# Optimization experiments

Measured on AMD Instinct MI355X. Metric: run time of the kernel, lower is better.

## Reference

```python
import jax, jax.numpy as jnp
import numpy as np

T, B, D, H = 512, 64, 512, 512

def setup_inputs() -> dict:
    key = jax.random.key(0)
    ks = jax.random.split(key, 14)
    s = 0.02
    inp = {
        "inputs": jax.random.normal(ks[0], (T, B, D), dtype=jnp.float32),
        # gate linears: weight [D+H, H] (transposed torch layout), bias [H]
        "Wf": jax.random.normal(ks[1], (D + H, H), dtype=jnp.float32) * s,
        "bf": jax.random.normal(ks[2], (H,), dtype=jnp.float32) * s,
        "Wi": jax.random.normal(ks[3], (D + H, H), dtype=jnp.float32) * s,
        "bi": jax.random.normal(ks[4], (H,), dtype=jnp.float32) * s,
        "Wg": jax.random.normal(ks[5], (D + H, H), dtype=jnp.float32) * s,
        "bg": jax.random.normal(ks[6], (H,), dtype=jnp.float32) * s,
        "Wo": jax.random.normal(ks[7], (D + H, H), dtype=jnp.float32) * s,
        "bo": jax.random.normal(ks[8], (H,), dtype=jnp.float32) * s,
        # residual linears on hidden state: [H, H], no bias
        "Rf": jax.random.normal(ks[9], (H, H), dtype=jnp.float32) * s,
        "Ri": jax.random.normal(ks[10], (H, H), dtype=jnp.float32) * s,
        "Rg": jax.random.normal(ks[11], (H, H), dtype=jnp.float32) * s,
        "Ro": jax.random.normal(ks[12], (H, H), dtype=jnp.float32) * s,
    }
    return inp


def reference(inputs, Wf, bf, Wi, bi, Wg, bg, Wo, bo, Rf, Ri, Rg, Ro):
    # QLSTM forward (eval mode, gate_dropout inactive). states=None -> zeros.
    batch = inputs.shape[1]
    hidden = Wf.shape[1]
    h0 = jnp.zeros((batch, hidden), dtype=inputs.dtype)
    c0 = jnp.zeros((batch, hidden), dtype=inputs.dtype)

    # Fuse the 4 gate GEMMs into one [D+H, 4H] matmul and the 4 residual
    # GEMMs into one [H, 4H] matmul (same math, fewer launches).
    W4 = jnp.concatenate([Wf, Wi, Wg, Wo], axis=1)   # [D+H, 4H]
    b4 = jnp.concatenate([bf, bi, bg, bo], axis=0)   # [4H]
    R4 = jnp.concatenate([Rf, Ri, Rg, Ro], axis=1)   # [H, 4H]

    def step(carry, x):
        hx, cx = carry
        combined = jnp.concatenate([x, hx], axis=1)            # [B, D+H]
        z = combined @ W4 + b4 + hx @ R4                        # [B, 4H]
        f, i, g, o = jnp.split(z, 4, axis=1)
        f = jax.nn.sigmoid(f)
        i = jax.nn.sigmoid(i)
        g = jnp.tanh(g)
        o = jax.nn.sigmoid(o)
        cx = f * cx + i * g
        hx = o * jnp.tanh(cx)
        return (hx, cx), hx

    (hx, cx), stacked = jax.lax.scan(step, (h0, c0), inputs)
    return stacked, hx, cx
```

## Files before the change

### kernel.cpp

```cpp
#include <hip/hip_runtime.h>
#include <hip/hip_bf16.h>

typedef __attribute__((ext_vector_type(8))) short s16x8;
typedef __attribute__((ext_vector_type(4))) float f32x4;

__device__ __forceinline__ ushort f2bf(float x) {
  __hip_bfloat16 b = __float2bfloat16(x);
  return *reinterpret_cast<ushort*>(&b);
}
__device__ __forceinline__ float bf2f(ushort u) {
  union { unsigned int i; float f; } c; c.i = ((unsigned int)u) << 16; return c.f;
}
__device__ __forceinline__ float sigm_fast(float z) {
  return __builtin_amdgcn_rcpf(1.0f + __builtin_amdgcn_exp2f(z * -1.44269504088896f));
}

__global__ __launch_bounds__(256) void pack_weights(
    const float* __restrict__ Wf, const float* __restrict__ Wi,
    const float* __restrict__ Wg, const float* __restrict__ Wo,
    const float* __restrict__ Rf, const float* __restrict__ Ri,
    const float* __restrict__ Rg, const float* __restrict__ Ro,
    const float* __restrict__ bfp, const float* __restrict__ bip,
    const float* __restrict__ bgp, const float* __restrict__ bop,
    ushort* __restrict__ Wx, ushort* __restrict__ Rs, float* __restrict__ bp)
{
  const int p = blockIdx.x * 8 + (threadIdx.x >> 5);
  const int kk = (threadIdx.x & 31) * 16;
  const int gate = p & 3;
  const int hcol = (p >> 5) * 8 + ((p >> 4) & 1) * 4 + ((p & 15) >> 2);
  const float* W = (gate == 0) ? Wf : (gate == 1) ? Wi : (gate == 2) ? Wg : Wo;
  const float* R = (gate == 0) ? Rf : (gate == 1) ? Ri : (gate == 2) ? Rg : Ro;
  union { ushort u[16]; s16x8 v[2]; } wb, rb;
#pragma unroll
  for (int e = 0; e < 16; ++e) {
    const int k = kk + e;
    wb.u[e] = f2bf(W[(size_t)k * 512 + hcol]);
    rb.u[e] = f2bf(W[(size_t)(512 + k) * 512 + hcol] + R[(size_t)k * 512 + hcol]);
  }
  *(s16x8*)(Wx + (size_t)p * 512 + kk)     = wb.v[0];
  *(s16x8*)(Wx + (size_t)p * 512 + kk + 8) = wb.v[1];
  *(s16x8*)(Rs + (size_t)p * 512 + kk)     = rb.v[0];
  *(s16x8*)(Rs + (size_t)p * 512 + kk + 8) = rb.v[1];
  if ((threadIdx.x & 31) == 0) {
    const float* B = (gate == 0) ? bfp : (gate == 1) ? bip : (gate == 2) ? bgp : bop;
    bp[p] = B[hcol];
  }
}

__global__ __launch_bounds__(512, 1) void fused_kernel(
    const float* __restrict__ x, const ushort* __restrict__ Wx,
    const ushort* __restrict__ Rs, const float* __restrict__ bp,
    const ushort* __restrict__ zxr, ushort* __restrict__ zxw,
    ushort* __restrict__ hbuf, float* __restrict__ csave,
    int* __restrict__ flags, ushort* __restrict__ hsave,
    float* __restrict__ cfinal, int t0, int CH, int zxt0, int do_rec)
{
  __shared__ ushort lds_u[33280];
  const int tid = threadIdx.x;
  const int wid = tid >> 6;
  const int lane = tid & 63;
  const int l15 = lane & 15;
  const int hi = lane >> 4;

  if (blockIdx.x >= 32) {
    if (zxt0 >= 512) return;
    const int zbid = blockIdx.x - 32;
    const int pg = zbid & 15;
    const int ts = zbid >> 4;
    const int mpair = wid >> 2;
    const int np = wid & 3;
    const int q = pg * 4 + np;
    s16x8 Bg[2][16];
#pragma unroll
    for (int nt = 0; nt < 2; ++nt)
#pragma unroll
      for (int kc = 0; kc < 16; ++kc)
        Bg[nt][kc] = *(const s16x8*)(Wx + (size_t)(q * 32 + nt * 16 + l15) * 512 + kc * 32 + hi * 8);
    const int tper = CH >> 3;
    for (int tt = 0; tt < tper; ++tt) {
      const int tl = ts * tper + tt;
      const int t = zxt0 + tl;
      const float4* x4 = (const float4*)(x + (size_t)t * 32768);
#pragma unroll
      for (int j = 0; j < 16; ++j) {
        const int i4 = j * 512 + tid;
        const float4 v = x4[i4];
        const int row = i4 >> 7;
        const int c0 = (i4 & 127) * 4;
        ushort4 u;
        u.x = f2bf(v.x); u.y = f2bf(v.y); u.z = f2bf(v.z); u.w = f2bf(v.w);
        *(ushort4*)(&lds_u[row * 520 + c0]) = u;
      }
      __syncthreads();
#pragma unroll
      for (int a = 0; a < 2; ++a) {
        const int mt = mpair * 2 + a;
        f32x4 a0 = {0.f, 0.f, 0.f, 0.f};
        f32x4 a1 = {0.f, 0.f, 0.f, 0.f};
#pragma unroll
        for (int kc = 0; kc < 16; ++kc) {
          const s16x8 af = *(const s16x8*)(&lds_u[(mt * 16 + l15) * 520 + kc * 32 + hi * 8]);
          a0 = __builtin_amdgcn_mfma_f32_16x16x32_bf16(af, Bg[0][kc], a0, 0, 0, 0);
          a1 = __builtin_amdgcn_mfma_f32_16x16x32_bf16(af, Bg[1][kc], a1, 0, 0, 0);
        }
        union { ushort u[8]; s16x8 v; } ub;
#pragma unroll
        for (int r = 0; r < 4; ++r) { ub.u[r] = f2bf(a0[r]); ub.u[4 + r] = f2bf(a1[r]); }
        *(s16x8*)(zxw + ((((size_t)tl * 4 + mt) * 64 + q) * 64 + lane) * 8) = ub.v;
      }
      __syncthreads();
    }
    return;
  }

  if (!do_rec) return;
  ushort* hsl = lds_u;
  ushort* tbuf = lds_u + 8192;
  const int bid = blockIdx.x;
  const int g = bid & 3;
  const int mem = bid >> 2;
  const int q = mem * 8 + wid;
  const int gate = lane & 3;

  f32x4 Brg[2][16];
#pragma unroll
  for (int nt = 0; nt < 2; ++nt)
#pragma unroll
    for (int kc = 0; kc < 16; ++kc) {
      Brg[nt][kc] = *(const f32x4*)(Rs + (size_t)(q * 32 + nt * 16 + l15) * 512 + kc * 32 + hi * 8);
      asm volatile("" : "+v"(Brg[nt][kc]));
    }
  const float b0 = bp[q * 32 + l15];
  const float b1 = bp[q * 32 + 16 + l15];

  float cst[2][4];
  float* csp = csave + ((size_t)(bid * 8 + wid) * 64 + lane) * 8;
  if (t0 == 0) {
#pragma unroll
    for (int i = 0; i < 2; ++i)
#pragma unroll
      for (int r = 0; r < 4; ++r) cst[i][r] = 0.0f;
  } else {
#pragma unroll
    for (int i = 0; i < 2; ++i)
#pragma unroll
      for (int r = 0; r < 4; ++r) cst[i][r] = csp[i * 4 + r];
  }

  const int srow = hi * 4 + gate;
  const int hcol0 = q * 8 + (l15 >> 2);
  const int crow = tid >> 5;
  const int cbyte = (tid & 31) * 32;
  const int cswz = (crow & 7) << 4;
  const int srcofs = crow * 512 + (cbyte >> 1);
  const int wofs0 = (crow * 1024 + (cbyte ^ cswz)) >> 1;
  const int wofs1 = (crow * 1024 + ((cbyte + 16) ^ cswz)) >> 1;
  const int abase = l15 * 1024 + hi * 16;
  const int aswz = (l15 & 7) << 4;
  int* const myflag = &flags[(g * 8 + mem) * 1024];
  int* const pollp = &flags[(g * 8 + (lane & 7)) * 1024];

  for (int tl = 0; tl < CH; ++tl) {
    const int t = t0 + tl;
    if (tl > 0) {
      asm volatile("s_waitcnt vmcnt(0)" ::: "memory");
      __syncthreads();
      if (tid == 0)
        __hip_atomic_store(myflag, t, __ATOMIC_RELAXED, __HIP_MEMORY_SCOPE_AGENT);
    }
    const s16x8 zv = *(const s16x8*)(zxr + ((((size_t)tl * 4 + g) * 64 + q) * 64 + lane) * 8);
    if (tl > 0) {
      int v = 0x7fffffff;
      if (lane < 8) v = __hip_atomic_load(pollp, __ATOMIC_RELAXED, __HIP_MEMORY_SCOPE_AGENT);
      while (!__all(v >= t)) {
        if (lane < 8) v = __hip_atomic_load(pollp, __ATOMIC_RELAXED, __HIP_MEMORY_SCOPE_AGENT);
      }
      asm volatile("" ::: "memory");
    }
    const ushort* hs = hbuf + ((size_t)tl * 4 + g) * 8192;
    const s16x8 h0 = *(const s16x8*)(hs + srcofs);
    const s16x8 h1 = *(const s16x8*)(hs + srcofs + 8);
    *(s16x8*)(&hsl[wofs0]) = h0;
    *(s16x8*)(&hsl[wofs1]) = h1;
    __syncthreads();
    f32x4 a0 = {0.f, 0.f, 0.f, 0.f};
    f32x4 a1 = {0.f, 0.f, 0.f, 0.f};
#pragma unroll
    for (int kc = 0; kc < 16; ++kc) {
      const s16x8 af = *(const s16x8*)(&hsl[((abase + kc * 64) ^ aswz) >> 1]);
      a0 = __builtin_amdgcn_mfma_f32_16x16x32_bf16(af, __builtin_bit_cast(s16x8, Brg[0][kc]), a0, 0, 0, 0);
      a1 = __builtin_amdgcn_mfma_f32_16x16x32_bf16(af, __builtin_bit_cast(s16x8, Brg[1][kc]), a1, 0, 0, 0);
    }
    float hv[2], cv[2];
#pragma unroll
    for (int nt = 0; nt < 2; ++nt) {
      float hr[4];
#pragma unroll
      for (int r = 0; r < 4; ++r) {
        float z = (nt ? a1[r] : a0[r]) + bf2f((ushort)zv[nt * 4 + r]) + (nt ? b1 : b0);
        const float zz = (gate == 2) ? z + z : z;
        const float s = sigm_fast(zz);
        const float act = (gate == 2) ? (s + s - 1.0f) : s;
        const int ai = __float_as_int(act);
        const float fv = __int_as_float(__builtin_amdgcn_mov_dpp(ai, 0x00, 0xF, 0xF, true));
        const float iv = __int_as_float(__builtin_amdgcn_mov_dpp(ai, 0x55, 0xF, 0xF, true));
        const float gv = __int_as_float(__builtin_amdgcn_mov_dpp(ai, 0xAA, 0xF, 0xF, true));
        const float ov = __int_as_float(__builtin_amdgcn_mov_dpp(ai, 0xFF, 0xF, 0xF, true));
        const float cn = fmaf(fv, cst[nt][r], iv * gv);
        cst[nt][r] = cn;
        const float s2 = sigm_fast(cn + cn);
        hr[r] = ov * (s2 + s2 - 1.0f);
      }
      hv[nt] = (gate == 0) ? hr[0] : (gate == 1) ? hr[1] : (gate == 2) ? hr[2] : hr[3];
      cv[nt] = (gate == 0) ? cst[nt][0] : (gate == 1) ? cst[nt][1]
             : (gate == 2) ? cst[nt][2] : cst[nt][3];
    }
    const ushort pb0 = f2bf(hv[0]), pb1 = f2bf(hv[1]);
    {
      ushort2 hp; hp.x = pb0; hp.y = pb1;
      *(ushort2*)(hsave + (((size_t)t * 4 + g) * 8 + mem) * 1024 + wid * 128 + lane * 2) = hp;
      if (t == 511) {
        float* cf = cfinal + (((size_t)(g * 8 + mem) * 8 + wid) * 64 + lane) * 2;
        cf[0] = cv[0]; cf[1] = cv[1];
      }
    }
    tbuf[wid * 128 + srow * 8 + (l15 >> 2)]     = pb0;
    tbuf[wid * 128 + srow * 8 + (l15 >> 2) + 4] = pb1;
    asm volatile("s_waitcnt lgkmcnt(0)" ::: "memory");
    __builtin_amdgcn_sched_barrier(0);
    if (tl != CH - 1) {
      if (lane < 16) {
        const unsigned long long* rp = (const unsigned long long*)&tbuf[wid * 128 + lane * 8];
        ushort* dst = hbuf + ((size_t)(tl + 1) * 4 + g) * 8192 + lane * 512 + q * 8;
        __hip_atomic_store((unsigned long long*)dst, rp[0],
                           __ATOMIC_RELAXED, __HIP_MEMORY_SCOPE_AGENT);
        __hip_atomic_store((unsigned long long*)(dst + 4), rp[1],
                           __ATOMIC_RELAXED, __HIP_MEMORY_SCOPE_AGENT);
      }
    } else {
      ushort* hn0 = hbuf + (size_t)g * 8192;
      hn0[srow * 512 + hcol0]     = pb0;
      hn0[srow * 512 + hcol0 + 4] = pb1;
    }
  }
#pragma unroll
  for (int i = 0; i < 2; ++i)
#pragma unroll
    for (int r = 0; r < 4; ++r) csp[i * 4 + r] = cst[i][r];
}

__global__ __launch_bounds__(256) void reorder_kernel(
    const ushort* __restrict__ hsave, const float* __restrict__ cfinal,
    float* __restrict__ dout)
{
  __shared__ ushort lds[8192];
  const int t = blockIdx.x;
  const int g = blockIdx.y;
  const int tid = threadIdx.x;
  const s16x8* src = (const s16x8*)(hsave + ((size_t)t * 4 + g) * 8192);
#pragma unroll
  for (int j = 0; j < 4; ++j) {
    const int i = j * 256 + tid;
    *(s16x8*)(&lds[i * 8]) = src[i];
  }
  __syncthreads();
  const int srow = tid >> 4;
  const int cb = (tid & 15) * 32;
  float buf[32];
#pragma unroll
  for (int cc = 0; cc < 32; ++cc) {
    const int col = cb + cc;
    const int q = col >> 3;
    const int memb = q >> 3;
    const int wd = q & 7;
    const int nt = (col >> 2) & 1;
    const int l15v = ((col & 3) << 2) | (srow & 3);
    const int lanev = ((srow >> 2) << 4) | l15v;
    buf[cc] = bf2f(lds[memb * 1024 + wd * 128 + lanev * 2 + nt]);
  }
  float* o = dout + (size_t)t * 32768 + (size_t)(g * 16 + srow) * 512 + cb;
#pragma unroll
  for (int j = 0; j < 8; ++j) *(float4*)(o + j * 4) = *(const float4*)(&buf[j * 4]);
  if (t == 511) {
    float* oh = dout + (size_t)16777216 + (size_t)(g * 16 + srow) * 512 + cb;
#pragma unroll
    for (int j = 0; j < 8; ++j) *(float4*)(oh + j * 4) = *(const float4*)(&buf[j * 4]);
    float cbuf[32];
#pragma unroll
    for (int cc = 0; cc < 32; ++cc) {
      const int col = cb + cc;
      const int q = col >> 3;
      const int memb = q >> 3;
      const int wd = q & 7;
      const int nt = (col >> 2) & 1;
      const int l15v = ((col & 3) << 2) | (srow & 3);
      const int lanev = ((srow >> 2) << 4) | l15v;
      cbuf[cc] = cfinal[(((size_t)(g * 8 + memb) * 8 + wd) * 64 + lanev) * 2 + nt];
    }
    float* oc = dout + (size_t)16809984 + (size_t)(g * 16 + srow) * 512 + cb;
#pragma unroll
    for (int j = 0; j < 8; ++j) *(float4*)(oc + j * 4) = *(const float4*)(&cbuf[j * 4]);
  }
}

extern "C" void kernel_launch(void* const* d_in, const int* in_sizes, int n_in,
                              void* d_out, int out_size, void* d_ws, size_t ws_size,
                              hipStream_t stream)
{
  const float* x   = (const float*)d_in[0];
  const float* Wf  = (const float*)d_in[1];
  const float* bfp = (const float*)d_in[2];
  const float* Wi  = (const float*)d_in[3];
  const float* bip = (const float*)d_in[4];
  const float* Wg  = (const float*)d_in[5];
  const float* bgp = (const float*)d_in[6];
  const float* Wo  = (const float*)d_in[7];
  const float* bop = (const float*)d_in[8];
  const float* Rf  = (const float*)d_in[9];
  const float* Ri  = (const float*)d_in[10];
  const float* Rg  = (const float*)d_in[11];
  const float* Ro  = (const float*)d_in[12];
  float* dout = (float*)d_out;
  char* ws = (char*)d_ws;

  const size_t o_Wx = 0;
  const size_t o_Rs = 2097152;
  const size_t o_bp = 4194304;
  const size_t o_z0 = o_bp + 8192;

  int CH = 64;
  for (;;) {
    const size_t need = o_z0 + 2 * (size_t)CH * 262144
                      + (size_t)(CH + 1) * 65536
                      + 524288 + 131072 + 33554432 + 131072;
    if (need <= ws_size || CH <= 8) break;
    CH >>= 1;
  }
  const size_t zsz  = (size_t)CH * 262144;
  const size_t o_z1 = o_z0 + zsz;
  const size_t o_hb = o_z1 + zsz;
  const size_t o_cs = o_hb + (size_t)(CH + 1) * 65536;
  const size_t o_fl = o_cs + 524288;
  const size_t o_hs = o_fl + 131072;
  const size_t o_cf = o_hs + 33554432;

  ushort* Wx   = (ushort*)(ws + o_Wx);
  ushort* Rs   = (ushort*)(ws + o_Rs);
  float*  bp   = (float*)(ws + o_bp);
  ushort* zx0  = (ushort*)(ws + o_z0);
  ushort* zx1  = (ushort*)(ws + o_z1);
  ushort* hb   = (ushort*)(ws + o_hb);
  float*  csv  = (float*)(ws + o_cs);
  int*    fl   = (int*)(ws + o_fl);
  ushort* hsv  = (ushort*)(ws + o_hs);
  float*  cfin = (float*)(ws + o_cf);

  pack_weights<<<256, 256, 0, stream>>>(Wf, Wi, Wg, Wo, Rf, Ri, Rg, Ro,
                                        bfp, bip, bgp, bop, Wx, Rs, bp);
  hipMemsetAsync(hb, 0, 65536, stream);
  hipMemsetAsync(fl, 0, 131072, stream);

  fused_kernel<<<160, 512, 0, stream>>>(x, Wx, Rs, bp, zx1, zx0, hb, csv, fl,
                                        hsv, cfin, 0, CH, 0, 0);
  const int nch = 512 / CH;
  for (int c = 0; c < nch; ++c) {
    const ushort* zr = (c & 1) ? zx1 : zx0;
    ushort* zw       = (c & 1) ? zx0 : zx1;
    fused_kernel<<<160, 512, 0, stream>>>(x, Wx, Rs, bp, zr, zw, hb, csv, fl,
                                          hsv, cfin, c * CH, CH, (c + 1) * CH, 1);
  }
  reorder_kernel<<<dim3(512, 4), 256, 0, stream>>>(hsv, cfin, dout);
}
```

Before: 1.715 ms.

## Process two batch groups per recurrent block, halving recurrent block count

Each recurrent block now handles two batch groups (A and B) in sequence each timestep, reusing the same register-resident recurrent weights. This drops the recurrent grid from 32 to 16 blocks. The aim is to interleave the two groups so the flag polling and latency of one group overlaps the compute of the other. The cost is twice the serial compute per block per step, plus two flag stores and two barriers per iteration.

```diff
diff --git a/kernel.cpp b/kernel.cpp
--- a/kernel.cpp
+++ b/kernel.cpp
@@ -62,9 +62,9 @@
   const int l15 = lane & 15;
   const int hi = lane >> 4;
 
-  if (blockIdx.x >= 32) {
+  if (blockIdx.x >= 16) {
     if (zxt0 >= 512) return;
-    const int zbid = blockIdx.x - 32;
+    const int zbid = blockIdx.x - 16;
     const int pg = zbid & 15;
     const int ts = zbid >> 4;
     const int mpair = wid >> 2;
@@ -114,11 +114,14 @@
   }
 
   if (!do_rec) return;
-  ushort* hsl = lds_u;
-  ushort* tbuf = lds_u + 8192;
+  ushort* hslA = lds_u;
+  ushort* hslB = lds_u + 8192;
+  ushort* tbuf = lds_u + 16384;
   const int bid = blockIdx.x;
-  const int g = bid & 3;
-  const int mem = bid >> 2;
+  const int team = bid >> 3;
+  const int mem = bid & 7;
+  const int gA = team * 2;
+  const int gB = team * 2 + 1;
   const int q = mem * 8 + wid;
   const int gate = lane & 3;
 
@@ -133,18 +136,18 @@
   const float b0 = bp[q * 32 + l15];
   const float b1 = bp[q * 32 + 16 + l15];
 
-  float cst[2][4];
-  float* csp = csave + ((size_t)(bid * 8 + wid) * 64 + lane) * 8;
+  float cA[2][4], cB[2][4];
+  float* csp = csave + ((size_t)(bid * 8 + wid) * 64 + lane) * 16;
   if (t0 == 0) {
 #pragma unroll
     for (int i = 0; i < 2; ++i)
 #pragma unroll
-      for (int r = 0; r < 4; ++r) cst[i][r] = 0.0f;
+      for (int r = 0; r < 4; ++r) { cA[i][r] = 0.0f; cB[i][r] = 0.0f; }
   } else {
 #pragma unroll
     for (int i = 0; i < 2; ++i)
 #pragma unroll
-      for (int r = 0; r < 4; ++r) cst[i][r] = csp[i * 4 + r];
+      for (int r = 0; r < 4; ++r) { cA[i][r] = csp[i * 4 + r]; cB[i][r] = csp[8 + i * 4 + r]; }
   }
 
   const int srow = hi * 4 + gate;
@@ -157,96 +160,108 @@
   const int wofs1 = (crow * 1024 + ((cbyte + 16) ^ cswz)) >> 1;
   const int abase = l15 * 1024 + hi * 16;
   const int aswz = (l15 & 7) << 4;
-  int* const myflag = &flags[(g * 8 + mem) * 1024];
-  int* const pollp = &flags[(g * 8 + (lane & 7)) * 1024];
+  int* const myflagA = &flags[(gA * 8 + mem) * 1024];
+  int* const myflagB = &flags[(gB * 8 + mem) * 1024];
+  int* const pollA = &flags[(gA * 8 + (lane & 7)) * 1024];
+  int* const pollB = &flags[(gB * 8 + (lane & 7)) * 1024];
+
+#define SECTION(G, HSL, CST, POLLP)                                              \
+  {                                                                              \
+    const s16x8 zv = *(const s16x8*)(zxr + ((((size_t)tl * 4 + (G)) * 64 + q) * 64 + lane) * 8); \
+    if (tl > 0) {                                                                \
+      int v = 0x7fffffff;                                                        \
+      if (lane < 8) v = __hip_atomic_load(POLLP, __ATOMIC_RELAXED, __HIP_MEMORY_SCOPE_AGENT); \
+      while (!__all(v >= t)) {                                                   \
+        if (lane < 8) v = __hip_atomic_load(POLLP, __ATOMIC_RELAXED, __HIP_MEMORY_SCOPE_AGENT); \
+      }                                                                          \
+      asm volatile("" ::: "memory");                                             \
+    }                                                                            \
+    const ushort* hs_ = hbuf + ((size_t)tl * 4 + (G)) * 8192;                    \
+    const s16x8 h0_ = *(const s16x8*)(hs_ + srcofs);                             \
+    const s16x8 h1_ = *(const s16x8*)(hs_ + srcofs + 8);                         \
+    *(s16x8*)(&HSL[wofs0]) = h0_;                                                \
+    *(s16x8*)(&HSL[wofs1]) = h1_;                                                \
+    __syncthreads();                                                             \
+    f32x4 a0_ = {0.f, 0.f, 0.f, 0.f};                                            \
+    f32x4 a1_ = {0.f, 0.f, 0.f, 0.f};                                            \
+    _Pragma("unroll")                                                            \
+    for (int kc = 0; kc < 16; ++kc) {                                            \
+      const s16x8 af_ = *(const s16x8*)(&HSL[((abase + kc * 64) ^ aswz) >> 1]);  \
+      a0_ = __builtin_amdgcn_mfma_f32_16x16x32_bf16(af_, __builtin_bit_cast(s16x8, Brg[0][kc]), a0_, 0, 0, 0); \
+      a1_ = __builtin_amdgcn_mfma_f32_16x16x32_bf16(af_, __builtin_bit_cast(s16x8, Brg[1][kc]), a1_, 0, 0, 0); \
+    }                                                                            \
+    float hv_[2], cv_[2];                                                        \
+    _Pragma("unroll")                                                            \
+    for (int nt = 0; nt < 2; ++nt) {                                             \
+      float hr_[4];                                                              \
+      _Pragma("unroll")                                                          \
+      for (int r = 0; r < 4; ++r) {                                              \
+        float z = (nt ? a1_[r] : a0_[r]) + bf2f((ushort)zv[nt * 4 + r]) + (nt ? b1 : b0); \
+        const float zz = (gate == 2) ? z + z : z;                                \
+        const float s = sigm_fast(zz);                                           \
+        const float act = (gate == 2) ? (s + s - 1.0f) : s;                      \
+        const int ai = __float_as_int(act);                                      \
+        const float fv = __int_as_float(__builtin_amdgcn_mov_dpp(ai, 0x00, 0xF, 0xF, true)); \
+        const float iv = __int_as_float(__builtin_amdgcn_mov_dpp(ai, 0x55, 0xF, 0xF, true)); \
+        const float gv = __int_as_float(__builtin_amdgcn_mov_dpp(ai, 0xAA, 0xF, 0xF, true)); \
+        const float ov = __int_as_float(__builtin_amdgcn_mov_dpp(ai, 0xFF, 0xF, 0xF, true)); \
+        const float cn = fmaf(fv, CST[nt][r], iv * gv);                          \
+        CST[nt][r] = cn;                                                         \
+        const float s2 = sigm_fast(cn + cn);                                     \
+        hr_[r] = ov * (s2 + s2 - 1.0f);                                          \
+      }                                                                          \
+      hv_[nt] = (gate == 0) ? hr_[0] : (gate == 1) ? hr_[1] : (gate == 2) ? hr_[2] : hr_[3]; \
+      cv_[nt] = (gate == 0) ? CST[nt][0] : (gate == 1) ? CST[nt][1]              \
+              : (gate == 2) ? CST[nt][2] : CST[nt][3];                           \
+    }                                                                            \
+    const ushort pb0 = f2bf(hv_[0]), pb1 = f2bf(hv_[1]);                         \
+    {                                                                            \
+      ushort2 hp; hp.x = pb0; hp.y = pb1;                                        \
+      *(ushort2*)(hsave + (((size_t)t * 4 + (G)) * 8 + mem) * 1024 + wid * 128 + lane * 2) = hp; \
+      if (t == 511) {                                                            \
+        float* cf = cfinal + (((size_t)((G) * 8 + mem) * 8 + wid) * 64 + lane) * 2; \
+        cf[0] = cv_[0]; cf[1] = cv_[1];                                          \
+      }                                                                          \
+    }                                                                            \
+    tbuf[wid * 128 + srow * 8 + (l15 >> 2)]     = pb0;                           \
+    tbuf[wid * 128 + srow * 8 + (l15 >> 2) + 4] = pb1;                           \
+    asm volatile("s_waitcnt lgkmcnt(0)" ::: "memory");                           \
+    __builtin_amdgcn_sched_barrier(0);                                           \
+    if (tl != CH - 1) {                                                          \
+      if (lane < 16) {                                                           \
+        const unsigned long long* rp = (const unsigned long long*)&tbuf[wid * 128 + lane * 8]; \
+        ushort* dst = hbuf + ((size_t)(tl + 1) * 4 + (G)) * 8192 + lane * 512 + q * 8; \
+        __hip_atomic_store((unsigned long long*)dst, rp[0],                      \
+                           __ATOMIC_RELAXED, __HIP_MEMORY_SCOPE_AGENT);          \
+        __hip_atomic_store((unsigned long long*)(dst + 4), rp[1],                \
+                           __ATOMIC_RELAXED, __HIP_MEMORY_SCOPE_AGENT);          \
+      }                                                                          \
+    } else {                                                                     \
+      ushort* hn0 = hbuf + (size_t)(G) * 8192;                                   \
+      hn0[srow * 512 + hcol0]     = pb0;                                         \
+      hn0[srow * 512 + hcol0 + 4] = pb1;                                         \
+    }                                                                            \
+  }
 
   for (int tl = 0; tl < CH; ++tl) {
     const int t = t0 + tl;
     if (tl > 0) {
       asm volatile("s_waitcnt vmcnt(0)" ::: "memory");
       __syncthreads();
-      if (tid == 0)
-        __hip_atomic_store(myflag, t, __ATOMIC_RELAXED, __HIP_MEMORY_SCOPE_AGENT);
-    }
-    const s16x8 zv = *(const s16x8*)(zxr + ((((size_t)tl * 4 + g) * 64 + q) * 64 + lane) * 8);
-    if (tl > 0) {
-      int v = 0x7fffffff;
-      if (lane < 8) v = __hip_atomic_load(pollp, __ATOMIC_RELAXED, __HIP_MEMORY_SCOPE_AGENT);
-      while (!__all(v >= t)) {
-        if (lane < 8) v = __hip_atomic_load(pollp, __ATOMIC_RELAXED, __HIP_MEMORY_SCOPE_AGENT);
-      }
-      asm volatile("" ::: "memory");
-    }
-    const ushort* hs = hbuf + ((size_t)tl * 4 + g) * 8192;
-    const s16x8 h0 = *(const s16x8*)(hs + srcofs);
-    const s16x8 h1 = *(const s16x8*)(hs + srcofs + 8);
-    *(s16x8*)(&hsl[wofs0]) = h0;
-    *(s16x8*)(&hsl[wofs1]) = h1;
-    __syncthreads();
-    f32x4 a0 = {0.f, 0.f, 0.f, 0.f};
-    f32x4 a1 = {0.f, 0.f, 0.f, 0.f};
-#pragma unroll
-    for (int kc = 0; kc < 16; ++kc) {
-      const s16x8 af = *(const s16x8*)(&hsl[((abase + kc * 64) ^ aswz) >> 1]);
-      a0 = __builtin_amdgcn_mfma_f32_16x16x32_bf16(af, __builtin_bit_cast(s16x8, Brg[0][kc]), a0, 0, 0, 0);
-      a1 = __builtin_amdgcn_mfma_f32_16x16x32_bf16(af, __builtin_bit_cast(s16x8, Brg[1][kc]), a1, 0, 0, 0);
-    }
-    float hv[2], cv[2];
-#pragma unroll
-    for (int nt = 0; nt < 2; ++nt) {
-      float hr[4];
-#pragma unroll
-      for (int r = 0; r < 4; ++r) {
-        float z = (nt ? a1[r] : a0[r]) + bf2f((ushort)zv[nt * 4 + r]) + (nt ? b1 : b0);
-        const float zz = (gate == 2) ? z + z : z;
-        const float s = sigm_fast(zz);
-        const float act = (gate == 2) ? (s + s - 1.0f) : s;
-        const int ai = __float_as_int(act);
-        const float fv = __int_as_float(__builtin_amdgcn_mov_dpp(ai, 0x00, 0xF, 0xF, true));
-        const float iv = __int_as_float(__builtin_amdgcn_mov_dpp(ai, 0x55, 0xF, 0xF, true));
-        const float gv = __int_as_float(__builtin_amdgcn_mov_dpp(ai, 0xAA, 0xF, 0xF, true));
-        const float ov = __int_as_float(__builtin_amdgcn_mov_dpp(ai, 0xFF, 0xF, 0xF, true));
-        const float cn = fmaf(fv, cst[nt][r], iv * gv);
-        cst[nt][r] = cn;
-        const float s2 = sigm_fast(cn + cn);
-        hr[r] = ov * (s2 + s2 - 1.0f);
-      }
-      hv[nt] = (gate == 0) ? hr[0] : (gate == 1) ? hr[1] : (gate == 2) ? hr[2] : hr[3];
-      cv[nt] = (gate == 0) ? cst[nt][0] : (gate == 1) ? cst[nt][1]
-             : (gate == 2) ? cst[nt][2] : cst[nt][3];
-    }
-    const ushort pb0 = f2bf(hv[0]), pb1 = f2bf(hv[1]);
-    {
-      ushort2 hp; hp.x = pb0; hp.y = pb1;
-      *(ushort2*)(hsave + (((size_t)t * 4 + g) * 8 + mem) * 1024 + wid * 128 + lane * 2) = hp;
-      if (t == 511) {
-        float* cf = cfinal + (((size_t)(g * 8 + mem) * 8 + wid) * 64 + lane) * 2;
-        cf[0] = cv[0]; cf[1] = cv[1];
+      if (tid == 0) {
+        __hip_atomic_store(myflagA, t, __ATOMIC_RELAXED, __HIP_MEMORY_SCOPE_AGENT);
+        __hip_atomic_store(myflagB, t, __ATOMIC_RELAXED, __HIP_MEMORY_SCOPE_AGENT);
       }
     }
-    tbuf[wid * 128 + srow * 8 + (l15 >> 2)]     = pb0;
-    tbuf[wid * 128 + srow * 8 + (l15 >> 2) + 4] = pb1;
-    asm volatile("s_waitcnt lgkmcnt(0)" ::: "memory");
-    __builtin_amdgcn_sched_barrier(0);
-    if (tl != CH - 1) {
-      if (lane < 16) {
-        const unsigned long long* rp = (const unsigned long long*)&tbuf[wid * 128 + lane * 8];
-        ushort* dst = hbuf + ((size_t)(tl + 1) * 4 + g) * 8192 + lane * 512 + q * 8;
-        __hip_atomic_store((unsigned long long*)dst, rp[0],
-                           __ATOMIC_RELAXED, __HIP_MEMORY_SCOPE_AGENT);
-        __hip_atomic_store((unsigned long long*)(dst + 4), rp[1],
-                           __ATOMIC_RELAXED, __HIP_MEMORY_SCOPE_AGENT);
-      }
-    } else {
-      ushort* hn0 = hbuf + (size_t)g * 8192;
-      hn0[srow * 512 + hcol0]     = pb0;
-      hn0[srow * 512 + hcol0 + 4] = pb1;
-    }
-  }
+    SECTION(gA, hslA, cA, pollA)
+    SECTION(gB, hslB, cB, pollB)
+  }
+#undef SECTION
+
 #pragma unroll
   for (int i = 0; i < 2; ++i)
 #pragma unroll
-    for (int r = 0; r < 4; ++r) csp[i * 4 + r] = cst[i][r];
+    for (int r = 0; r < 4; ++r) { csp[i * 4 + r] = cA[i][r]; csp[8 + i * 4 + r] = cB[i][r]; }
 }
 
 __global__ __launch_bounds__(256) void reorder_kernel(
@@ -360,13 +375,13 @@
   hipMemsetAsync(hb, 0, 65536, stream);
   hipMemsetAsync(fl, 0, 131072, stream);
 
-  fused_kernel<<<160, 512, 0, stream>>>(x, Wx, Rs, bp, zx1, zx0, hb, csv, fl,
+  fused_kernel<<<144, 512, 0, stream>>>(x, Wx, Rs, bp, zx1, zx0, hb, csv, fl,
                                         hsv, cfin, 0, CH, 0, 0);
   const int nch = 512 / CH;
   for (int c = 0; c < nch; ++c) {
     const ushort* zr = (c & 1) ? zx1 : zx0;
     ushort* zw       = (c & 1) ? zx0 : zx1;
-    fused_kernel<<<160, 512, 0, stream>>>(x, Wx, Rs, bp, zr, zw, hb, csv, fl,
+    fused_kernel<<<144, 512, 0, stream>>>(x, Wx, Rs, bp, zr, zw, hb, csv, fl,
                                           hsv, cfin, c * CH, CH, (c + 1) * CH, 1);
   }
   reorder_kernel<<<dim3(512, 4), 256, 0, stream>>>(hsv, cfin, dout);
```

New measurement: 3.032 ms. 1.77x slower.
